# Optimization experiments

Measured on AMD Instinct MI355X. Metric: run time of the kernel, lower is better.

Reference implementation:

```python
import jax, jax.numpy as jnp
import numpy as np

B, S, D, H, F = 2, 2048, 1024, 16, 4096
HD = D // H
EPS = 1e-5


def _layernorm(x, g, b):
    mu = jnp.mean(x, axis=-1, keepdims=True)
    var = jnp.var(x, axis=-1, keepdims=True)
    return (x - mu) * jax.lax.rsqrt(var + EPS) * g + b


def setup_inputs() -> dict:
    key = jax.random.key(0)
    ks = jax.random.split(key, 10)
    sd = 0.02
    return {
        "src": jax.random.normal(ks[0], (B, S, D), jnp.float32),
        "qkv_w": jax.random.normal(ks[1], (3 * D, D), jnp.float32) * sd,
        "qkv_b": jnp.zeros((3 * D,), jnp.float32),
        "out_w": jax.random.normal(ks[2], (D, D), jnp.float32) * sd,
        "out_b": jnp.zeros((D,), jnp.float32),
        "ffn_w1": jax.random.normal(ks[3], (F, D), jnp.float32) * sd,
        "ffn_b1": jnp.zeros((F,), jnp.float32),
        "ffn_w2": jax.random.normal(ks[4], (D, F), jnp.float32) * sd,
        "ffn_b2": jnp.zeros((D,), jnp.float32),
        "ln1_g": jnp.ones((D,), jnp.float32),
        "ln1_b": jnp.zeros((D,), jnp.float32),
        "ln2_g": jnp.ones((D,), jnp.float32),
        "ln2_b": jnp.zeros((D,), jnp.float32),
    }


def reference(src, qkv_w, qkv_b, out_w, out_b, ffn_w1, ffn_b1, ffn_w2, ffn_b2,
              ln1_g, ln1_b, ln2_g, ln2_b):
    # --- Multi-head self-attention (post-norm, dropout=identity in eval) ---
    qkv = src @ qkv_w.T + qkv_b                        # [B,S,3D]
    qkv = qkv.reshape(B, S, H, 3 * HD).transpose(0, 2, 1, 3)  # [B,H,S,3hd]
    q, k, v = jnp.split(qkv, 3, axis=-1)               # each [B,H,S,hd]
    scores = jnp.einsum('bhqd,bhkd->bhqk', q, k) / np.sqrt(HD).astype(np.float32)
    attn = jax.nn.softmax(scores, axis=-1)
    ctx = jnp.einsum('bhqk,bhkd->bhqd', attn, v)       # [B,H,S,hd]
    ctx = ctx.transpose(0, 2, 1, 3).reshape(B, S, D)
    mha_out = ctx @ out_w.T + out_b
    agg = _layernorm(src + mha_out, ln1_g, ln1_b)
    # --- FFN: Linear -> ReLU -> Linear ---
    h = jax.nn.relu(agg @ ffn_w1.T + ffn_b1)
    ffn_out = h @ ffn_w2.T + ffn_b2
    return _layernorm(agg + ffn_out, ln2_g, ln2_b)
```

## Files before the change

### kernel.cpp

```cpp
#include <hip/hip_runtime.h>


typedef unsigned short u16;
typedef unsigned int u32;
typedef __attribute__((ext_vector_type(8))) __bf16 bf16x8;
typedef __attribute__((ext_vector_type(4))) float f32x4;
typedef __attribute__((ext_vector_type(4))) short s16x4;
typedef __attribute__((ext_vector_type(2))) u32 u32x2;

__device__ __forceinline__ u16 f2bf(float f) {
  u32 u = __float_as_uint(f);
  u += 0x7fffu + ((u >> 16) & 1u);
  return (u16)(u >> 16);
}

__device__ __forceinline__ float bf2f(u16 h) {
  return __uint_as_float((u32)h << 16);
}

__device__ __forceinline__ u32 pk_bf_trunc(float a, float b) {
  return (__float_as_uint(a) >> 16) | (__float_as_uint(b) & 0xffff0000u);
}

__device__ __forceinline__ float exp2_fast(float x) {
  float t = __builtin_fmaf(x, 8388608.0f, 1064992506.0f);
  return __int_as_float((int)t);
}

__device__ __forceinline__ void async16(const void* g, void* l) {
  __builtin_amdgcn_global_load_lds((__attribute__((address_space(1))) void*)g,
                                   (__attribute__((address_space(3))) void*)l,
                                   16, 0, 0);
}

__device__ __forceinline__ f32x4 mfma16(bf16x8 a, bf16x8 b, f32x4 c) {
  return __builtin_amdgcn_mfma_f32_16x16x32_bf16(a, b, c, 0, 0, 0);
}

__device__ __forceinline__ f32x4 mfma_pv(s16x4 a, s16x4 b, f32x4 c) {
#if __has_builtin(__builtin_amdgcn_mfma_f32_16x16x16bf16_1k)
  return __builtin_amdgcn_mfma_f32_16x16x16bf16_1k(a, b, c, 0, 0, 0);
#else
  f32x4 d;
  asm("v_mfma_f32_16x16x16_bf16 %0, %1, %2, %3" : "=v"(d) : "v"(a), "v"(b), "v"(c));
  return d;
#endif
}

__global__ __launch_bounds__(256)
void cvt_all(const float* __restrict__ qkv_w, const float* __restrict__ out_w,
             const float* __restrict__ f1, const float* __restrict__ f2,
             const float* __restrict__ src,
             u16* __restrict__ o_qkv, u16* __restrict__ o_out,
             u16* __restrict__ o_f1, u16* __restrict__ o_f2,
             u16* __restrict__ o_src) {
  int b = blockIdx.x;
  const float* in;
  u16* out;
  int lb, ob;
  if (b < 3072) {
    int h = b / 192, c = b - h * 192;
    ob = (c < 64) ? h * 64 + c : (c < 128) ? 1024 + h * 64 + (c - 64)
                                           : 2048 + h * 64 + (c - 128);
    in = qkv_w; out = o_qkv; lb = b;
  }
  else if (b < 4096)  { in = out_w; out = o_out; lb = b - 3072;  ob = lb; }
  else if (b < 8192)  { in = f1;    out = o_f1;  lb = b - 4096;  ob = lb; }
  else if (b < 12288) { in = f2;    out = o_f2;  lb = b - 8192;  ob = lb; }
  else                { in = src;   out = o_src; lb = b - 12288; ob = lb; }
  int i = lb * 256 + threadIdx.x;
  int o = ob * 256 + threadIdx.x;
  float4 v = ((const float4*)in)[i];
  ushort4 ov;
  ov.x = f2bf(v.x); ov.y = f2bf(v.y); ov.z = f2bf(v.z); ov.w = f2bf(v.w);
  ((ushort4*)out)[o] = ov;
}

template <int MODE, int SPLIT>
__global__ __launch_bounds__(256)
void gemm_bt(const u16* __restrict__ A, const u16* __restrict__ W,
             const float* __restrict__ bias,
             u16* __restrict__ outb,
             u16* __restrict__ qo, u16* __restrict__ ko, u16* __restrict__ vto,
             int M, int N, int K) {
  __shared__ u16 As[128 * 64];
  __shared__ u16 Bs[128 * 64];
  const int lane = threadIdx.x & 63;
  const int wave = threadIdx.x >> 6;
  const int lrow = lane & 15;
  const int lq = lane >> 4;
  const int tm = blockIdx.x * 128;
  const int tn = blockIdx.y * 128;
  const int wm = (wave >> 1) * 64;
  const int wn = (wave & 1) * 64;
  const int kc = K / SPLIT;
  const int kbeg = blockIdx.z * kc;
  f32x4 acc[4][4] = {};

  for (int k0 = kbeg; k0 < kbeg + kc; k0 += 64) {
#pragma unroll
    for (int c = 0; c < 4; ++c) {
      int chunk = wave * 256 + c * 64 + lane;
      int row = chunk >> 3;
      int sc = chunk & 7;
      int cc = sc ^ (row & 7);
      u16* la = As + (size_t)(wave * 256 + c * 64) * 8;
      u16* lb = Bs + (size_t)(wave * 256 + c * 64) * 8;
      async16(A + (size_t)(tm + row) * K + (k0 + cc * 8), la);
      async16(W + (size_t)(tn + row) * K + (k0 + cc * 8), lb);
    }
    __syncthreads();
#pragma unroll
    for (int h = 0; h < 2; ++h) {
      bf16x8 a_frag[4], b_frag[4];
#pragma unroll
      for (int i = 0; i < 4; ++i) {
        int row = wm + i * 16 + lrow;
        int sc = (h * 4 + lq) ^ (row & 7);
        a_frag[i] = *(const bf16x8*)(As + row * 64 + sc * 8);
      }
#pragma unroll
      for (int j = 0; j < 4; ++j) {
        int row = wn + j * 16 + lrow;
        int sc = (h * 4 + lq) ^ (row & 7);
        b_frag[j] = *(const bf16x8*)(Bs + row * 64 + sc * 8);
      }
#pragma unroll
      for (int i = 0; i < 4; ++i)
#pragma unroll
        for (int j = 0; j < 4; ++j)
          acc[i][j] = mfma16(a_frag[i], b_frag[j], acc[i][j]);
    }
    __syncthreads();
  }

  if constexpr (MODE == 2) {
    const int type = tn >> 10;
    if (type < 2) {
      u16* dst = (type == 0) ? qo : ko;
      const float scale = (type == 0) ? 0.1803368801f : 1.f;
#pragma unroll
      for (int j = 0; j < 4; ++j) {
        int idx = (tn & 1023) + wn + j * 16 + lrow;
        int hh = idx >> 6, c = idx & 63;
        float bv = bias[hh * 192 + type * 64 + c];
#pragma unroll
        for (int i = 0; i < 4; ++i) {
#pragma unroll
          for (int r = 0; r < 4; ++r) {
            int row = tm + wm + i * 16 + lq * 4 + r;
            int b = row >> 11, s = row & 2047;
            dst[(((size_t)(b * 16 + hh) * 2048 + s) << 6) + c] =
                f2bf((acc[i][j][r] + bv) * scale);
          }
        }
      }
    } else {
#pragma unroll
      for (int j = 0; j < 4; ++j) {
        int idx = (tn & 1023) + wn + j * 16 + lrow;
        int hh = idx >> 6, c = idx & 63;
        float bv = bias[hh * 192 + 128 + c];
#pragma unroll
        for (int i = 0; i < 4; ++i) {
          int row0 = tm + wm + i * 16 + lq * 4;
          int b = row0 >> 11, s0 = row0 & 2047;
          ushort4 pk;
          pk.x = f2bf(acc[i][j][0] + bv);
          pk.y = f2bf(acc[i][j][1] + bv);
          pk.z = f2bf(acc[i][j][2] + bv);
          pk.w = f2bf(acc[i][j][3] + bv);
          *(ushort4*)(vto + (((size_t)(b * 16 + hh) * 64 + c) << 11) + s0) = pk;
        }
      }
    }
    return;
  }

  u16* outp = outb;
  if constexpr (MODE == 0) outp += (size_t)blockIdx.z * M * N;

#pragma unroll
  for (int i = 0; i < 4; ++i) {
#pragma unroll
    for (int j = 0; j < 4; ++j) {
      int col = tn + wn + j * 16 + lrow;
      float bv = (SPLIT == 1 || blockIdx.z == 0) ? bias[col] : 0.f;
#pragma unroll
      for (int r = 0; r < 4; ++r) {
        int row = tm + wm + i * 16 + lq * 4 + r;
        float v = acc[i][j][r] + bv;
        if constexpr (MODE == 0) {
          outp[(size_t)row * N + col] = f2bf(v);
        } else {
          outp[(size_t)row * N + col] = f2bf(fmaxf(v, 0.f));
        }
      }
    }
  }
}

__global__ __launch_bounds__(512)
void attn_kernel(const u16* __restrict__ Q, const u16* __restrict__ K,
                 const u16* __restrict__ Vt,
                 u16* __restrict__ o_part, float* __restrict__ l_part) {
  __shared__ u16 Ks[128 * 64];
  __shared__ u16 Vs[64 * 128];
  const int tid = threadIdx.x;
  const int lane = tid & 63;
  const int wave = tid >> 6;
  const int wq = wave & 3;
  const int half = wave >> 2;
  const int lrow = lane & 15;
  const int q = lane >> 4;
  const int bh = blockIdx.x & 31;
  const int qb = (blockIdx.x >> 5) & 15;
  const int kvh = blockIdx.x >> 9;
  const u16* Qp = Q + ((size_t)bh * 2048 + qb * 128 + half * 64) * 64;
  const u16* Kp = K + (size_t)bh * 2048 * 64;
  const u16* Vp = Vt + (size_t)bh * 64 * 2048;

  bf16x8 qf[2];
#pragma unroll
  for (int kk = 0; kk < 2; ++kk)
    qf[kk] = *(const bf16x8*)(Qp + (wq * 16 + lrow) * 64 + kk * 32 + q * 8);

  const s16x4 ones = {(short)0x3F80, (short)0x3F80, (short)0x3F80, (short)0x3F80};
  f32x4 oacc[4] = {};
  f32x4 lacc = {};

  for (int kb = kvh * 8; kb < kvh * 8 + 8; ++kb) {
    if (half == 0) {
#pragma unroll
      for (int t = 0; t < 4; ++t) {
        int c = wq * 256 + t * 64 + lane;
        int row = c >> 3, sc = c & 7;
        int cc = sc ^ (row & 7);
        async16(Kp + (size_t)(kb * 128 + row) * 64 + cc * 8,
                Ks + (size_t)(wq * 256 + t * 64) * 8);
      }
    } else {
#pragma unroll
      for (int t = 0; t < 4; ++t) {
        int c = wq * 256 + t * 64 + lane;
        int row = c >> 4, sc = c & 15;
        int cc = sc ^ (row & 7);
        async16(Vp + (size_t)row * 2048 + kb * 128 + cc * 8,
                Vs + (size_t)(wq * 256 + t * 64) * 8);
      }
    }
    __syncthreads();

    f32x4 sacc[8] = {};
#pragma unroll
    for (int j = 0; j < 8; ++j) {
#pragma unroll
      for (int kk = 0; kk < 2; ++kk) {
        int row = j * 16 + lrow;
        int sc = (kk * 4 + q) ^ (row & 7);
        bf16x8 kf = *(const bf16x8*)(Ks + row * 64 + sc * 8);
        sacc[j] = mfma16(kf, qf[kk], sacc[j]);
      }
    }

    s16x4 pa[8];
#pragma unroll
    for (int j = 0; j < 8; ++j) {
      float p0 = exp2_fast(sacc[j][0]);
      float p1 = exp2_fast(sacc[j][1]);
      float p2 = exp2_fast(sacc[j][2]);
      float p3 = exp2_fast(sacc[j][3]);
      u32x2 pw;
      pw.x = pk_bf_trunc(p0, p1);
      pw.y = pk_bf_trunc(p2, p3);
      pa[j] = __builtin_bit_cast(s16x4, pw);
    }

#pragma unroll
    for (int j = 0; j < 8; ++j) {
      lacc = mfma_pv(pa[j], ones, lacc);
#pragma unroll
      for (int jn = 0; jn < 4; ++jn) {
        int row = jn * 16 + lrow;
        int sc = (j * 2 + (q >> 1)) ^ (row & 7);
        s16x4 vb = *(const s16x4*)(Vs + row * 128 + sc * 8 + (q & 1) * 4);
        oacc[jn] = mfma_pv(pa[j], vb, oacc[jn]);
      }
    }
    __syncthreads();
  }

  const int b = bh >> 4, h = bh & 15;
  u16* op = o_part + (size_t)kvh * 4096 * 1024;
  float* lp = l_part + kvh * 65536 + bh * 2048;
#pragma unroll
  for (int r = 0; r < 4; ++r) {
    int s = qb * 128 + half * 64 + wq * 16 + q * 4 + r;
    if (lrow == 0) lp[s] = lacc[r];
    size_t base = ((size_t)(b * 2048 + s)) * 1024 + h * 64;
#pragma unroll
    for (int jn = 0; jn < 4; ++jn)
      op[base + jn * 16 + lrow] = f2bf(oacc[jn][r]);
  }
}

__global__ __launch_bounds__(256)
void attn_combine(const u16* __restrict__ o_part, const float* __restrict__ l_part,
                  u16* __restrict__ ctx) {
  const int t = blockIdx.x;
  const int tid = threadIdx.x;
  __shared__ float linv[16];
  if (tid < 16) {
    int b = t >> 11, s = t & 2047;
    int bh = b * 16 + tid;
    linv[tid] = 1.f / (l_part[bh * 2048 + s] + l_part[65536 + bh * 2048 + s]);
  }
  __syncthreads();
  size_t base = (size_t)t * 1024;
  ushort4 a = ((const ushort4*)(o_part + base))[tid];
  ushort4 c = ((const ushort4*)(o_part + 4096ull * 1024 + base))[tid];
  float li = linv[tid >> 4];
  ushort4 o;
  o.x = f2bf((bf2f(a.x) + bf2f(c.x)) * li);
  o.y = f2bf((bf2f(a.y) + bf2f(c.y)) * li);
  o.z = f2bf((bf2f(a.z) + bf2f(c.z)) * li);
  o.w = f2bf((bf2f(a.w) + bf2f(c.w)) * li);
  ((ushort4*)(ctx + base))[tid] = o;
}

template <int P>
__global__ __launch_bounds__(256)
void ln_kernel(const float* __restrict__ x1, const u16* __restrict__ x2,
               const float* __restrict__ g, const float* __restrict__ bb,
               float* __restrict__ outf, u16* __restrict__ outb) {
  const int t = blockIdx.x;
  const int tid = threadIdx.x;
  const int lane = tid & 63, wave = tid >> 6;
  const size_t base = (size_t)t * 1024;
  const size_t pstride = 4096ull * 1024;
  float v[4];
  float s = 0.f, s2 = 0.f;
#pragma unroll
  for (int e = 0; e < 4; ++e) {
    int i = tid + e * 256;
    float x = x1[base + i];
#pragma unroll
    for (int p = 0; p < P; ++p) x += bf2f(x2[p * pstride + base + i]);
    v[e] = x;
    s += x;
    s2 += x * x;
  }
#pragma unroll
  for (int d = 1; d < 64; d <<= 1) {
    s += __shfl_xor(s, d);
    s2 += __shfl_xor(s2, d);
  }
  __shared__ float red[8];
  if (lane == 0) { red[wave] = s; red[4 + wave] = s2; }
  __syncthreads();
  s = red[0] + red[1] + red[2] + red[3];
  s2 = red[4] + red[5] + red[6] + red[7];
  float mean = s * (1.f / 1024.f);
  float var = s2 * (1.f / 1024.f) - mean * mean;
  float rstd = rsqrtf(var + 1e-5f);
#pragma unroll
  for (int e = 0; e < 4; ++e) {
    int i = tid + e * 256;
    float y = (v[e] - mean) * rstd * g[i] + bb[i];
    outf[base + i] = y;
    if (outb) outb[base + i] = f2bf(y);
  }
}

extern "C" void kernel_launch(void* const* d_in, const int* in_sizes, int n_in,
                              void* d_out, int out_size, void* d_ws, size_t ws_size,
                              hipStream_t stream) {
  const float* src    = (const float*)d_in[0];
  const float* qkv_w  = (const float*)d_in[1];
  const float* qkv_b  = (const float*)d_in[2];
  const float* out_w  = (const float*)d_in[3];
  const float* out_b  = (const float*)d_in[4];
  const float* ffn_w1 = (const float*)d_in[5];
  const float* ffn_b1 = (const float*)d_in[6];
  const float* ffn_w2 = (const float*)d_in[7];
  const float* ffn_b2 = (const float*)d_in[8];
  const float* ln1_g  = (const float*)d_in[9];
  const float* ln1_b  = (const float*)d_in[10];
  const float* ln2_g  = (const float*)d_in[11];
  const float* ln2_b  = (const float*)d_in[12];

  char* ws = (char*)d_ws;
  size_t off = 0;
  auto alloc = [&](size_t bytes) -> void* {
    void* p = ws + off;
    off += (bytes + 255) & ~(size_t)255;
    return p;
  };
  u16* wqkv = (u16*)alloc(3072ull * 1024 * 2);
  u16* wout = (u16*)alloc(1024ull * 1024 * 2);
  u16* wf1  = (u16*)alloc(4096ull * 1024 * 2);
  u16* wf2  = (u16*)alloc(1024ull * 4096 * 2);
  u16* srcb = (u16*)alloc(4096ull * 1024 * 2);
  u16* qb_  = (u16*)alloc(32ull * 2048 * 64 * 2);
  u16* kb_  = (u16*)alloc(32ull * 2048 * 64 * 2);
  u16* vtb  = (u16*)alloc(32ull * 64 * 2048 * 2);
  u16* opart = (u16*)alloc(2ull * 4096 * 1024 * 2);
  float* lpart = (float*)alloc(2ull * 65536 * 4);
  u16* ctxb = (u16*)alloc(4096ull * 1024 * 2);
  u16* mha  = (u16*)alloc(4ull * 4096 * 1024 * 2);
  float* aggf = (float*)alloc(4096ull * 1024 * 4);
  u16* aggb = (u16*)alloc(4096ull * 1024 * 2);
  u16* hb   = (u16*)alloc(4096ull * 4096 * 2);
  u16* ffnf = (u16*)alloc(4ull * 4096 * 1024 * 2);

  cvt_all<<<16384, 256, 0, stream>>>(qkv_w, out_w, ffn_w1, ffn_w2, src,
                                     wqkv, wout, wf1, wf2, srcb);

  gemm_bt<2, 1><<<dim3(32, 24), 256, 0, stream>>>(srcb, wqkv, qkv_b, nullptr,
                                                  qb_, kb_, vtb, 4096, 3072, 1024);
  attn_kernel<<<1024, 512, 0, stream>>>(qb_, kb_, vtb, opart, lpart);
  attn_combine<<<4096, 256, 0, stream>>>(opart, lpart, ctxb);
  gemm_bt<0, 4><<<dim3(32, 8, 4), 256, 0, stream>>>(ctxb, wout, out_b, mha,
                                                    nullptr, nullptr, nullptr, 4096, 1024, 1024);
  ln_kernel<4><<<4096, 256, 0, stream>>>(src, mha, ln1_g, ln1_b, aggf, aggb);
  gemm_bt<1, 1><<<dim3(32, 32), 256, 0, stream>>>(aggb, wf1, ffn_b1, hb,
                                                  nullptr, nullptr, nullptr, 4096, 4096, 1024);
  gemm_bt<0, 4><<<dim3(32, 8, 4), 256, 0, stream>>>(hb, wf2, ffn_b2, ffnf,
                                                    nullptr, nullptr, nullptr, 4096, 1024, 4096);
  ln_kernel<4><<<4096, 256, 0, stream>>>(aggf, ffnf, ln2_g, ln2_b, (float*)d_out, nullptr);
}
```

Before: 373.1 us.

## Process 256 query rows per attention block to reuse K/V tiles

Each attention block now covers 256 query rows instead of 128. Every one of the 8 waves handles two 16-row query slices against the same shared K/V tile, and the grid is halved. This halves global K/V loads and LDS fill work per query and amortizes the barriers. The cost is doubled accumulator registers and fewer blocks (512), which may reduce occupancy on a 256-CU device.

```diff
diff --git a/kernel.cpp b/kernel.cpp
--- a/kernel.cpp
+++ b/kernel.cpp
@@ -210,27 +210,30 @@
   const int lane = tid & 63;
   const int wave = tid >> 6;
   const int wq = wave & 3;
-  const int half = wave >> 2;
+  const int role = wave >> 2;
   const int lrow = lane & 15;
   const int q = lane >> 4;
   const int bh = blockIdx.x & 31;
-  const int qb = (blockIdx.x >> 5) & 15;
-  const int kvh = blockIdx.x >> 9;
-  const u16* Qp = Q + ((size_t)bh * 2048 + qb * 128 + half * 64) * 64;
+  const int qb = (blockIdx.x >> 5) & 7;
+  const int kvh = blockIdx.x >> 8;
+  const u16* Qp = Q + ((size_t)bh * 2048 + qb * 256) * 64;
   const u16* Kp = K + (size_t)bh * 2048 * 64;
   const u16* Vp = Vt + (size_t)bh * 64 * 2048;
 
-  bf16x8 qf[2];
-#pragma unroll
-  for (int kk = 0; kk < 2; ++kk)
-    qf[kk] = *(const bf16x8*)(Qp + (wq * 16 + lrow) * 64 + kk * 32 + q * 8);
+  bf16x8 qf[2][2];
+#pragma unroll
+  for (int h2 = 0; h2 < 2; ++h2)
+#pragma unroll
+    for (int kk = 0; kk < 2; ++kk)
+      qf[h2][kk] = *(const bf16x8*)(Qp + (h2 * 128 + wave * 16 + lrow) * 64 +
+                                    kk * 32 + q * 8);
 
   const s16x4 ones = {(short)0x3F80, (short)0x3F80, (short)0x3F80, (short)0x3F80};
-  f32x4 oacc[4] = {};
-  f32x4 lacc = {};
+  f32x4 oacc[2][4] = {};
+  f32x4 lacc[2] = {};
 
   for (int kb = kvh * 8; kb < kvh * 8 + 8; ++kb) {
-    if (half == 0) {
+    if (role == 0) {
 #pragma unroll
       for (int t = 0; t < 4; ++t) {
         int c = wq * 256 + t * 64 + lane;
@@ -251,40 +254,43 @@
     }
     __syncthreads();
 
-    f32x4 sacc[8] = {};
-#pragma unroll
-    for (int j = 0; j < 8; ++j) {
-#pragma unroll
-      for (int kk = 0; kk < 2; ++kk) {
-        int row = j * 16 + lrow;
-        int sc = (kk * 4 + q) ^ (row & 7);
-        bf16x8 kf = *(const bf16x8*)(Ks + row * 64 + sc * 8);
-        sacc[j] = mfma16(kf, qf[kk], sacc[j]);
-      }
-    }
-
-    s16x4 pa[8];
-#pragma unroll
-    for (int j = 0; j < 8; ++j) {
-      float p0 = exp2_fast(sacc[j][0]);
-      float p1 = exp2_fast(sacc[j][1]);
-      float p2 = exp2_fast(sacc[j][2]);
-      float p3 = exp2_fast(sacc[j][3]);
-      u32x2 pw;
-      pw.x = pk_bf_trunc(p0, p1);
-      pw.y = pk_bf_trunc(p2, p3);
-      pa[j] = __builtin_bit_cast(s16x4, pw);
-    }
-
-#pragma unroll
-    for (int j = 0; j < 8; ++j) {
-      lacc = mfma_pv(pa[j], ones, lacc);
-#pragma unroll
-      for (int jn = 0; jn < 4; ++jn) {
-        int row = jn * 16 + lrow;
-        int sc = (j * 2 + (q >> 1)) ^ (row & 7);
-        s16x4 vb = *(const s16x4*)(Vs + row * 128 + sc * 8 + (q & 1) * 4);
-        oacc[jn] = mfma_pv(pa[j], vb, oacc[jn]);
+#pragma unroll
+    for (int h2 = 0; h2 < 2; ++h2) {
+      f32x4 sacc[8] = {};
+#pragma unroll
+      for (int j = 0; j < 8; ++j) {
+#pragma unroll
+        for (int kk = 0; kk < 2; ++kk) {
+          int row = j * 16 + lrow;
+          int sc = (kk * 4 + q) ^ (row & 7);
+          bf16x8 kf = *(const bf16x8*)(Ks + row * 64 + sc * 8);
+          sacc[j] = mfma16(kf, qf[h2][kk], sacc[j]);
+        }
+      }
+
+      s16x4 pa[8];
+#pragma unroll
+      for (int j = 0; j < 8; ++j) {
+        float p0 = exp2_fast(sacc[j][0]);
+        float p1 = exp2_fast(sacc[j][1]);
+        float p2 = exp2_fast(sacc[j][2]);
+        float p3 = exp2_fast(sacc[j][3]);
+        u32x2 pw;
+        pw.x = pk_bf_trunc(p0, p1);
+        pw.y = pk_bf_trunc(p2, p3);
+        pa[j] = __builtin_bit_cast(s16x4, pw);
+      }
+
+#pragma unroll
+      for (int j = 0; j < 8; ++j) {
+        lacc[h2] = mfma_pv(pa[j], ones, lacc[h2]);
+#pragma unroll
+        for (int jn = 0; jn < 4; ++jn) {
+          int row = jn * 16 + lrow;
+          int sc = (j * 2 + (q >> 1)) ^ (row & 7);
+          s16x4 vb = *(const s16x4*)(Vs + row * 128 + sc * 8 + (q & 1) * 4);
+          oacc[h2][jn] = mfma_pv(pa[j], vb, oacc[h2][jn]);
+        }
       }
     }
     __syncthreads();
@@ -294,13 +300,16 @@
   u16* op = o_part + (size_t)kvh * 4096 * 1024;
   float* lp = l_part + kvh * 65536 + bh * 2048;
 #pragma unroll
-  for (int r = 0; r < 4; ++r) {
-    int s = qb * 128 + half * 64 + wq * 16 + q * 4 + r;
-    if (lrow == 0) lp[s] = lacc[r];
-    size_t base = ((size_t)(b * 2048 + s)) * 1024 + h * 64;
-#pragma unroll
-    for (int jn = 0; jn < 4; ++jn)
-      op[base + jn * 16 + lrow] = f2bf(oacc[jn][r]);
+  for (int h2 = 0; h2 < 2; ++h2) {
+#pragma unroll
+    for (int r = 0; r < 4; ++r) {
+      int s = qb * 256 + h2 * 128 + wave * 16 + q * 4 + r;
+      if (lrow == 0) lp[s] = lacc[h2][r];
+      size_t base = ((size_t)(b * 2048 + s)) * 1024 + h * 64;
+#pragma unroll
+      for (int jn = 0; jn < 4; ++jn)
+        op[base + jn * 16 + lrow] = f2bf(oacc[h2][jn][r]);
+    }
   }
 }
 
@@ -418,7 +427,7 @@
 
   gemm_bt<2, 1><<<dim3(32, 24), 256, 0, stream>>>(srcb, wqkv, qkv_b, nullptr,
                                                   qb_, kb_, vtb, 4096, 3072, 1024);
-  attn_kernel<<<1024, 512, 0, stream>>>(qb_, kb_, vtb, opart, lpart);
+  attn_kernel<<<512, 512, 0, stream>>>(qb_, kb_, vtb, opart, lpart);
   attn_combine<<<4096, 256, 0, stream>>>(opart, lpart, ctxb);
   gemm_bt<0, 4><<<dim3(32, 8, 4), 256, 0, stream>>>(ctxb, wout, out_b, mha,
                                                     nullptr, nullptr, nullptr, 4096, 1024, 1024);
```

Measured after the change: 371.8 us. Within noise of the previous version (-0.3%).
